# Optimization experiments

Measured on AMD Instinct MI355X. Metric: run time of the kernel, lower is better.

The kernel has to match this reference:

```python
import jax, jax.numpy as jnp
import numpy as np

STRIDE = 16
SIZES = np.array([128.0, 256.0, 512.0], np.float32)
RATIOS = np.array([0.5, 1.0, 2.0], np.float32)
N_POS, N_NEG = 32, 32          # n_sample=64, pos_ratio=0.5
POS_THR, NEG_THR = 0.7, 0.2
W_CONF, W_REG = 1.0, 5.0


def _conv(x, w, b, stride, pad):
    y = jax.lax.conv_general_dilated(x, w, (stride, stride), [(pad, pad), (pad, pad)],
                                     dimension_numbers=('NCHW', 'OIHW', 'NCHW'))
    return y + b[None, :, None, None]


def _anchors(fw, fh, stride):
    # 9 anchors per center: 3 sizes x 3 aspect ratios
    ws = (SIZES[:, None] * np.sqrt(RATIOS)[None, :]).reshape(-1)
    hs = (SIZES[:, None] / np.sqrt(RATIOS)[None, :]).reshape(-1)
    wh = jnp.asarray(np.stack([ws, hs], -1))                      # (9,2)
    cx = (jnp.arange(fw, dtype=jnp.float32) + 0.5) * stride
    cy = (jnp.arange(fh, dtype=jnp.float32) + 0.5) * stride
    gx, gy = jnp.meshgrid(cx, cy, indexing='ij')                  # x-major, like the torch list comp
    ctr = jnp.stack([gx, gy], -1)[:, :, None, :]                  # (fw,fh,1,2)
    tl = ctr - wh / 2.0
    xywh = jnp.concatenate([tl, jnp.broadcast_to(wh, tl.shape)], -1)  # (fw,fh,9,4)
    return xywh.reshape(-1, 4)


def _xywh_to_xyxy(b):
    return jnp.concatenate([b[:, :2], b[:, :2] + b[:, 2:]], -1)


def _iou(a, b):  # a [N,4], b [M,4], xyxy
    lt = jnp.maximum(a[:, None, :2], b[None, :, :2])
    rb = jnp.minimum(a[:, None, 2:], b[None, :, 2:])
    inter = jnp.clip(rb - lt, 0.0).prod(-1)
    aa = (a[:, 2] - a[:, 0]) * (a[:, 3] - a[:, 1])
    ab = (b[:, 2] - b[:, 0]) * (b[:, 3] - b[:, 1])
    return inter / (aa[:, None] + ab[None, :] - inter)


def _head_flat(y, per):  # [1, 9*per, H, W] -> [W*H*9, per], matching anchor flatten order
    _, _, H, W = y.shape
    return y[0].reshape(9, per, H, W).transpose(3, 2, 0, 1).reshape(-1, per)


def _apply_offsets(boxes, off):  # decode proposals from xyxy boxes + (dx,dy,dw,dh)
    w = boxes[:, 2] - boxes[:, 0]; h = boxes[:, 3] - boxes[:, 1]
    cx = boxes[:, 0] + 0.5 * w;    cy = boxes[:, 1] + 0.5 * h
    ncx = cx + off[:, 0] * w;      ncy = cy + off[:, 1] * h
    nw = w * jnp.exp(off[:, 2]);   nh = h * jnp.exp(off[:, 3])
    return jnp.stack([ncx - nw / 2, ncy - nh / 2, ncx + nw / 2, ncy + nh / 2], -1)


def _box_offset(anc, gt):
    aw = anc[:, 2] - anc[:, 0]; ah = anc[:, 3] - anc[:, 1]
    acx = anc[:, 0] + 0.5 * aw; acy = anc[:, 1] + 0.5 * ah
    gw = gt[:, 2] - gt[:, 0];   gh = gt[:, 3] - gt[:, 1]
    gcx = gt[:, 0] + 0.5 * gw;  gcy = gt[:, 1] + 0.5 * gh
    return jnp.stack([(gcx - acx) / aw, (gcy - acy) / ah,
                      jnp.log(gw / aw), jnp.log(gh / ah)], -1)


def setup_inputs():
    key = jax.random.key(0)
    ks = jax.random.split(key, 12)
    img_data = jax.random.normal(ks[0], (1, 3, 1600, 1600), jnp.float32)
    x1 = jax.random.uniform(ks[1], (64,), minval=0.0, maxval=1400.0)
    y1 = jax.random.uniform(ks[2], (64,), minval=0.0, maxval=1400.0)
    bw = jax.random.uniform(ks[3], (64,), minval=32.0, maxval=200.0)
    bh = jax.random.uniform(ks[4], (64,), minval=32.0, maxval=200.0)
    gt_boxes = jnp.stack([x1, y1, x1 + bw, y1 + bh], -1)[None]   # [1,64,4], all valid (no -1 pad)
    gt_classes = jax.random.randint(ks[5], (1, 64), 1, 21, jnp.int32)
    def w(k, shape, fan):
        return jax.random.normal(k, shape, jnp.float32) * np.float32(np.sqrt(2.0 / fan))
    return dict(
        img_data=img_data, gt_boxes=gt_boxes, gt_classes=gt_classes,
        w1=w(ks[6], (64, 3, 7, 7), 3 * 49),      b1=jnp.zeros(64, jnp.float32),
        w2=w(ks[7], (256, 64, 3, 3), 64 * 9),    b2=jnp.zeros(256, jnp.float32),
        w_rpn=w(ks[8], (256, 256, 3, 3), 256 * 9), b_rpn=jnp.zeros(256, jnp.float32),
        w_cls=w(ks[9], (18, 256, 1, 1), 256),    b_cls=jnp.zeros(18, jnp.float32),
        w_reg=w(ks[10], (36, 256, 1, 1), 256),   b_reg=jnp.zeros(36, jnp.float32),
    )


def reference(img_data, gt_boxes, gt_classes, w1, b1, w2, b2, w_rpn, b_rpn, w_cls, b_cls, w_reg, b_reg):
    # --- feature extractor (total stride 16) ---
    fm = jax.nn.relu(_conv(img_data, w1, b1, 4, 3))
    fm = jax.nn.relu(_conv(fm, w2, b2, 4, 1))            # [1,256,100,100]
    H, W = fm.shape[2], fm.shape[3]
    # --- anchors + IoU matching ---
    anchors_xywh = _anchors(W, H, STRIDE)                # [N,4] xywh
    anchors_xyxy = _xywh_to_xyxy(anchors_xywh)
    gt = gt_boxes[0]                                     # [M,4], all valid
    ious = _iou(anchors_xyxy, gt)                        # [N,M]
    N = ious.shape[0]
    gt_max = ious.max(0)                                 # best iou per gt
    is_gt_best = (ious == gt_max[None, :]).any(1)        # torch: where(iou == gt_max)[0]
    anc_argmax = ious.argmax(1)
    anc_max = ious.max(1)
    labels = jnp.full((N,), -1.0, jnp.float32)
    labels = jnp.where(anc_max < NEG_THR, 0.0, labels)
    labels = jnp.where(is_gt_best, 1.0, labels)
    labels = jnp.where(anc_max > POS_THR, 1.0, labels)
    # --- deterministic pos/neg sampling (fixed sizes; replaces randperm subsampling) ---
    idx = jnp.arange(N, dtype=jnp.float32)
    _, pos_index = jax.lax.top_k(jnp.where(labels == 1.0, anc_max, -1.0), N_POS)
    _, neg_index = jax.lax.top_k(jnp.where(labels == 0.0, 1e6 - idx, -1e9), N_NEG)
    bboxes_pos = anchors_xyxy[pos_index]                 # box_convert(xywh->xyxy) of pos anchors
    # --- proposal module (RPN head) ---
    h = jax.nn.relu(_conv(fm, w_rpn, b_rpn, 1, 1))
    cls = _head_flat(_conv(h, w_cls, b_cls, 1, 0), 2)    # [N,2]
    reg = _head_flat(_conv(h, w_reg, b_reg, 1, 0), 4)    # [N,4]
    pos_score = cls[pos_index]
    neg_score = cls[neg_index]
    offset_pos = reg[pos_index]
    proposals = _apply_offsets(bboxes_pos, offset_pos)
    # --- losses ---
    gt_offset = _box_offset(bboxes_pos, gt[anc_argmax[pos_index]])
    logits = jnp.concatenate([pos_score, neg_score], 0)  # [64,2]
    tgt = jnp.concatenate([jnp.ones(N_POS, jnp.int32), jnp.zeros(N_NEG, jnp.int32)])
    logp = jax.nn.log_softmax(logits, -1)
    cls_loss = -logp[jnp.arange(N_POS + N_NEG), tgt].mean()
    d = gt_offset - offset_pos
    ad = jnp.abs(d)
    reg_loss = jnp.where(ad < 1.0, 0.5 * d * d, ad - 0.5).mean()
    total_rpn_loss = W_CONF * cls_loss + W_REG * reg_loss
    gt_cls_pos = gt_classes[0][anc_argmax[pos_index]]
    return (total_rpn_loss, fm, proposals, pos_index, gt_cls_pos)
```

## Files before the change

kernel.cpp:

```cpp
#include <hip/hip_runtime.h>
#include <math.h>


#define CAP 4096

typedef __attribute__((ext_vector_type(8))) short bf16x8;
typedef __attribute__((ext_vector_type(4))) float f32x4;

__device__ __forceinline__ void dma16(const void* g, void* l) {
    __builtin_amdgcn_global_load_lds((const __attribute__((address_space(1))) void*)g,
                                     (__attribute__((address_space(3))) void*)l, 16, 0, 0);
}

#define OFF_F1T     0
#define OFF_FMT     5171328
#define OFF_CPART   6503040
#define OFF_RPART   7223040
#define OFF_WA1     8663040
#define OFF_W9_2    8672448
#define OFF_W9_3    8746176
#define OFF_WTC     9041088
#define OFF_WTG     9045696
#define OFF_AARG    9054912
#define OFF_NEGM    9144912
#define OFF_POSM    9147728
#define OFF_GTMAX   9150544
#define OFF_CANDS   9150688
#define OFF_CANDI   9154784
#define OFF_IMGB    9158880

__device__ __forceinline__ unsigned short f2bf(float f) {
    unsigned int u = __float_as_uint(f);
    u += 0x7fffu + ((u >> 16) & 1u);
    return (unsigned short)(u >> 16);
}

__device__ __forceinline__ void anchor_box(int i, float& x0, float& y0,
                                           float& x1, float& y1, float& area) {
#pragma clang fp contract(off)
    const float sizes[3]  = {128.f, 256.f, 512.f};
    const float ratios[3] = {0.5f, 1.f, 2.f};
    int a = i % 9;
    int q = i / 9;
    int iy = q % 100;
    int ix = q / 100;
    int s = a / 3, r = a % 3;
    float sq = sqrtf(ratios[r]);
    float w = sizes[s] * sq;
    float h = sizes[s] / sq;
    float cx = ((float)ix + 0.5f) * 16.0f;
    float cy = ((float)iy + 0.5f) * 16.0f;
    x0 = cx - w * 0.5f;
    y0 = cy - h * 0.5f;
    x1 = x0 + w;
    y1 = y0 + h;
    area = (x1 - x0) * (y1 - y0);
}

__device__ __forceinline__ float iou_one(float ax0, float ay0, float ax1, float ay1, float aa,
                                         float bx0, float by0, float bx1, float by1, float ab) {
#pragma clang fp contract(off)
    float ltx = fmaxf(ax0, bx0), lty = fmaxf(ay0, by0);
    float rbx = fminf(ax1, bx1), rby = fminf(ay1, by1);
    float iw = fmaxf(rbx - ltx, 0.0f);
    float ih = fmaxf(rby - lty, 0.0f);
    float inter = iw * ih;
    return inter / ((aa + ab) - inter);
}

__global__ __launch_bounds__(256) void setup_kernel(const float* __restrict__ wc, float* __restrict__ wtc,
                                                    const float* __restrict__ wg, float* __restrict__ wtg,
                                                    const float* __restrict__ w1, unsigned short* __restrict__ wa1,
                                                    const float* __restrict__ w2, unsigned short* __restrict__ w9_2,
                                                    const float* __restrict__ wr, unsigned short* __restrict__ w9_3,
                                                    unsigned int* __restrict__ f1t_u, unsigned int* __restrict__ fmt_u,
                                                    unsigned int* __restrict__ gtmax,
                                                    const float* __restrict__ img, unsigned short* __restrict__ imgb) {
    int i = blockIdx.x * 256 + threadIdx.x;
    if (i < 65) { gtmax[i] = 0u; return; }
    i -= 65;
    if (i < 103040) {
        if (i < 51328) {
            int p = i >> 5, part = i & 31;
            int x, y;
            if (p < 804) { y = (p < 402) ? 0 : 401; x = p % 402; }
            else { int j = p - 804; x = (j < 400) ? 0 : 401; y = 1 + (j % 400); }
            f1t_u[(y * 402 + x) * 32 + part] = 0u;
        } else {
            int i2 = i - 51328;
            int p = i2 >> 7, part = i2 & 127;
            int x, y;
            if (p < 204) { y = (p < 102) ? 0 : 101; x = p % 102; }
            else { int j = p - 204; x = (j < 100) ? 0 : 101; y = 1 + (j % 100); }
            fmt_u[(y * 102 + x) * 128 + part] = 0u;
        }
        return;
    }
    i -= 103040;
    if (i < 4608) { int c = i / 256, k = i - c * 256; wtc[k * 18 + c] = wc[i]; return; }
    i -= 4608;
    if (i < 9216) { int c = i / 256, k = i - c * 256; wtg[k * 36 + c] = wg[i]; return; }
    i -= 9216;
    if (i < 12288) {
        int oc = i / 192, k = i - oc * 192;
        int q = k >> 3, kx = k & 7;
        int ky = q / 3, ic = q - (q / 3) * 3;
        wa1[i] = (q < 21 && kx < 7) ? f2bf(w1[oc * 147 + ic * 49 + ky * 7 + kx])
                                    : (unsigned short)0;
        return;
    }
    i -= 12288;
    if (i < 147456) {
        int unit = i >> 13;
        int rem = i & 8191;
        int ocT = rem >> 9;
        int rem2 = rem & 511;
        int lane = rem2 >> 3;
        int e = rem2 & 7;
        int cc = unit >> 1, kcl = unit & 1;
        int oc = ocT * 16 + (lane & 15);
        int ic = kcl * 32 + (lane >> 4) * 8 + e;
        w9_2[i] = f2bf(w2[(oc * 64 + ic) * 9 + cc]);
        return;
    }
    i -= 147456;
    if (i < 589824) {
        int unit = i >> 13;
        int rem = i & 8191;
        int ocT = rem >> 9;
        int rem2 = rem & 511;
        int lane = rem2 >> 3;
        int e = rem2 & 7;
        int cc = unit >> 1, kcl = unit & 1;
        int kk = cc >> 2, chv = cc & 3;
        int oc = ocT * 16 + (lane & 15);
        int icl = kcl * 32 + (lane >> 4) * 8 + e;
        w9_3[i] = f2bf(wr[(oc * 256 + chv * 64 + icl) * 9 + kk]);
        return;
    }
    i -= 589824;
    if (i < 7680000) {
        int ic = i / 2560000;
        int rem = i - ic * 2560000;
        int y = rem / 1600, x = rem - (rem / 1600) * 1600;
        imgb[((size_t)(ic * 1608 + y + 3)) * 1608 + x + 3] = f2bf(img[((size_t)(ic * 1600 + y)) * 1600 + x]);
        return;
    }
    i -= 7680000;
    if (i < 38592) {
        int ic = i / 12864;
        int rem = i - ic * 12864;
        int r8 = rem / 1608, xp = rem - r8 * 1608;
        int yp = (r8 < 3) ? r8 : (1600 + r8);
        imgb[((size_t)(ic * 1608 + yp)) * 1608 + xp] = 0;
        return;
    }
    i -= 38592;
    if (i < 28800) {
        int ic = i / 9600;
        int rem = i - ic * 9600;
        int y = rem / 6, xi = rem - (rem / 6) * 6;
        int xp = (xi < 3) ? xi : (1602 + xi);
        imgb[((size_t)(ic * 1608 + y + 3)) * 1608 + xp] = 0;
    }
}

__device__ __forceinline__ void iou1_body(int bid, int t, const float* __restrict__ gt,
                                          int* __restrict__ aarg, unsigned int* __restrict__ gtmax) {
    __shared__ float sg1[64][4];
    __shared__ float sarea1[64];
    __shared__ unsigned int smax1[64];
    if (t < 64) {
#pragma clang fp contract(off)
        float b0 = gt[t * 4 + 0], b1 = gt[t * 4 + 1];
        float b2 = gt[t * 4 + 2], b3 = gt[t * 4 + 3];
        sg1[t][0] = b0; sg1[t][1] = b1; sg1[t][2] = b2; sg1[t][3] = b3;
        sarea1[t] = (b2 - b0) * (b3 - b1);
        smax1[t] = 0u;
    }
    __syncthreads();
    int i = bid * 256 + t;
    int iq = min(i, 89999);
    float x0, y0, x1, y1, aa;
    anchor_box(iq, x0, y0, x1, y1, aa);
    float best = -1.f;
    int bestj = 0;
    for (int j = 0; j < 64; j++) {
        float v = iou_one(x0, y0, x1, y1, aa, sg1[j][0], sg1[j][1], sg1[j][2], sg1[j][3], sarea1[j]);
        if (v > best) { best = v; bestj = j; }
        float vm = v;
#pragma unroll
        for (int off = 32; off > 0; off >>= 1) vm = fmaxf(vm, __shfl_xor(vm, off));
        if ((t & 63) == 0) atomicMax(&smax1[j], __float_as_uint(vm));
    }
    if (i < 90000) aarg[i] = bestj;
    __syncthreads();
    if (t < 64) atomicMax(&gtmax[t], smax1[t]);
}

__device__ __forceinline__ void iou2_body(int bid, int t, const float* __restrict__ gt,
                                          const unsigned int* __restrict__ gtmax,
                                          unsigned long long* __restrict__ negmask,
                                          unsigned long long* __restrict__ posmask,
                                          float* __restrict__ cand_s, int* __restrict__ cand_i,
                                          unsigned int* __restrict__ cnt) {
    __shared__ float sg2[64][4];
    __shared__ float sarea2[64];
    __shared__ float sgm2[64];
    if (t < 64) {
#pragma clang fp contract(off)
        float b0 = gt[t * 4 + 0], b1 = gt[t * 4 + 1];
        float b2 = gt[t * 4 + 2], b3 = gt[t * 4 + 3];
        sg2[t][0] = b0; sg2[t][1] = b1; sg2[t][2] = b2; sg2[t][3] = b3;
        sarea2[t] = (b2 - b0) * (b3 - b1);
        sgm2[t] = __uint_as_float(gtmax[t]);
    }
    __syncthreads();
    int i = bid * 512 + t;
    if (i >= 90000) return;
    float x0, y0, x1, y1, aa;
    anchor_box(i, x0, y0, x1, y1, aa);
    float best = -1.f;
    bool isbest = false;
    for (int j = 0; j < 64; j++) {
        float v = iou_one(x0, y0, x1, y1, aa, sg2[j][0], sg2[j][1], sg2[j][2], sg2[j][3], sarea2[j]);
        if (v > best) best = v;
        if (v == sgm2[j]) isbest = true;
    }
    float label = -1.f;
    if (best < 0.2f) label = 0.f;
    if (isbest) label = 1.f;
    if (best > 0.7f) label = 1.f;
    unsigned long long negb = __ballot(label == 0.f);
    unsigned long long posb = __ballot(label == 1.f);
    if ((t & 63) == 0) { negmask[i >> 6] = negb; posmask[i >> 6] = posb; }
    if (label == 1.f) {
        unsigned int p = atomicAdd(cnt, 1u);
        if (p < CAP) { cand_s[p] = best; cand_i[p] = i; }
    }
}

__device__ __forceinline__ void conv1_body(int bx, int oy, int t,
                                           const unsigned short* __restrict__ imgb,
                                           const unsigned short* __restrict__ wA,
                                           const float* __restrict__ bias,
                                           unsigned short* __restrict__ f1t) {
    __shared__ __align__(16) unsigned char smem[13312];
    unsigned short* win = (unsigned short*)smem;
    unsigned short* tileT = (unsigned short*)smem;
    int wave = t >> 6, lane = t & 63;
    int quad = lane >> 4, l16 = lane & 15;
    int ox0 = bx * 64;
    int col0 = ox0 * 4;
    int gy0 = 4 * oy - 3;
    const size_t ZROW = ((size_t)(2 * 1608 + 1606)) * 1608;

    for (int o = wave; o < 13; o += 4) {
        int q = o * 64 + lane;
        int r = q / 33;
        int c = q - r * 33;
        int rc = min(r, 20);
        int ky = rc / 3, ic = rc - (rc / 3) * 3;
        int yp = gy0 + ky + 3;
        size_t offm = ((size_t)(ic * 1608 + yp)) * 1608 + col0 + c * 8;
        size_t offz = ZROW + (size_t)(q - 693) * 8;
        dma16(imgb + ((r < 21) ? offm : offz), (char*)smem + o * 1024);
    }
    bf16x8 afr[6];
    {
        const bf16x8* ap = (const bf16x8*)(wA + (wave * 16 + l16) * 192 + quad * 8);
#pragma unroll
        for (int c = 0; c < 6; c++) afr[c] = ap[c * 4];
    }
    __syncthreads();

    f32x4 acc[4];
#pragma unroll
    for (int j = 0; j < 4; j++) acc[j] = (f32x4){0.f, 0.f, 0.f, 0.f};
#pragma unroll
    for (int ch = 0; ch < 6; ch++) {
        const unsigned short* wrow = win + (ch * 4 + quad) * 264;
#pragma unroll
        for (int j = 0; j < 4; j++) {
            int px = j * 16 + l16;
            const unsigned long long* bp = (const unsigned long long*)(wrow + 4 * px);
            union { unsigned long long u[2]; bf16x8 v; } uu;
            uu.u[0] = bp[0];
            uu.u[1] = bp[1];
            acc[j] = __builtin_amdgcn_mfma_f32_16x16x32_bf16(afr[ch], uu.v, acc[j], 0, 0, 0);
        }
    }
    __syncthreads();
#pragma unroll
    for (int reg = 0; reg < 4; reg++) {
        int oc = wave * 16 + quad * 4 + reg;
        float bv = bias[oc];
#pragma unroll
        for (int j = 0; j < 4; j++) {
            int px = j * 16 + l16;
            tileT[px * 72 + oc] = f2bf(fmaxf(acc[j][reg] + bv, 0.f));
        }
    }
    __syncthreads();
    int px = t >> 2, part = t & 3;
    int ox = ox0 + px;
    if (ox < 400) {
        int row = (oy + 1) * 402 + ox + 1;
        uint4 v0 = *(const uint4*)(tileT + px * 72 + part * 16);
        uint4 v1 = *(const uint4*)(tileT + px * 72 + part * 16 + 8);
        *(uint4*)(f1t + row * 64 + part * 16) = v0;
        *(uint4*)(f1t + row * 64 + part * 16 + 8) = v1;
    }
}

__global__ __launch_bounds__(256, 4) void conv1_iou1(const unsigned short* __restrict__ imgb,
                                                     const unsigned short* __restrict__ wA,
                                                     const float* __restrict__ bias,
                                                     unsigned short* __restrict__ f1t,
                                                     const float* __restrict__ gt,
                                                     int* __restrict__ aarg,
                                                     unsigned int* __restrict__ gtmax) {
    int t = threadIdx.x;
    if (blockIdx.x < 7) {
        conv1_body(blockIdx.x, blockIdx.y, t, imgb, wA, bias, f1t);
    } else {
        int bid = blockIdx.y;
        if (bid < 352) iou1_body(bid, t, gt, aarg, gtmax);
    }
}

template<int ICC, int RS, int S, bool WRT, bool HEAD>
__device__ __forceinline__ void conv_body(int xs, int y, int t,
                                          const unsigned short* __restrict__ Bt,
                                          const unsigned short* __restrict__ A9,
                                          const float* __restrict__ bias,
                                          float* __restrict__ outF,
                                          unsigned short* __restrict__ outT,
                                          const float* __restrict__ wtc,
                                          const float* __restrict__ wtg,
                                          float* __restrict__ cpart,
                                          float* __restrict__ rpart) {
    constexpr int NC = ICC / 64;
    constexpr int HC = S * 24 + 3;
    constexpr int CHW = ICC / 8;
    constexpr int TOT = 3 * HC * CHW;
    constexpr int BOPS = (TOT + 63) / 64;
    constexpr int BB = BOPS * 1024;
    constexpr int NS = (NC == 1) ? 18 : 72;
    __shared__ __align__(16) unsigned char smem[BB + 32768];
    unsigned short* blds = (unsigned short*)smem;
    float* hlds = (float*)(smem + BB);

    int wave = t >> 6, lane = t & 63;
    int ow = wave & 3, ph = wave >> 2;
    int quad = lane >> 4, l16 = lane & 15;
    int oc0 = ow * 64;
    int pl = ph * 16 + l16;
    int pxe = min(pl, 24);
    int swp = pxe & 7;

    for (int o = wave; o < BOPS; o += 8) {
        int q = min(o * 64 + lane, TOT - 1);
        int row = q / CHW;
        int e = q - row * CHW;
        int ky = row / HC;
        int c = row - ky * HC;
        int sz = (S == 4) ? (e ^ ((c >> 2) & 7)) : (e ^ (row & 7));
        dma16(Bt + ((size_t)(S * y + ky) * RS + S * xs * 25 + c) * ICC + sz * 8,
              (char*)smem + o * 1024);
    }
    for (int o = wave; o < 16; o += 8)
        dma16(A9 + (size_t)(o * 64 + lane) * 8, (char*)smem + BB + o * 1024);

    f32x4 acc[4];
#pragma unroll
    for (int mt = 0; mt < 4; mt++) acc[mt] = (f32x4){0.f, 0.f, 0.f, 0.f};
    __syncthreads();

    for (int u = 0; u < NS; u++) {
        if (u + 1 < NS) {
            char* dst = (char*)smem + BB + ((u + 1) & 1) * 16384;
            const unsigned short* src = A9 + (size_t)(u + 1) * 8192;
            for (int o = wave; o < 16; o += 8)
                dma16(src + (size_t)(o * 64 + lane) * 8, dst + o * 1024);
        }
        const unsigned short* ab = (const unsigned short*)(smem + BB + (u & 1) * 16384);
        int cc = u >> 1, kcl = u & 1;
        int pass = cc / NC, ch = cc - pass * NC;
        int ky = pass / 3, kx = pass - (pass / 3) * 3;
        int row = ky * HC + S * pxe + kx;
        int ck = kcl * 4 + quad;
        int chunk = (S == 4) ? (ck ^ swp) : ((ch * 8 + ck) ^ (row & 7));
        bf16x8 bf = *(const bf16x8*)(blds + row * ICC + chunk * 8);
#pragma unroll
        for (int mt = 0; mt < 4; mt++) {
            bf16x8 af = *(const bf16x8*)(ab + ((ow * 4 + mt) * 64 + lane) * 8);
            acc[mt] = __builtin_amdgcn_mfma_f32_16x16x32_bf16(af, bf, acc[mt], 0, 0, 0);
        }
        __syncthreads();
    }

#pragma unroll
    for (int mt = 0; mt < 4; mt++) {
#pragma unroll
        for (int reg = 0; reg < 4; reg++) {
            int oc = oc0 + mt * 16 + quad * 4 + reg;
            float bv = bias[oc];
            if (pl < 25) {
                float v = fmaxf(acc[mt][reg] + bv, 0.f);
                if (HEAD) {
                    hlds[oc * 26 + pl] = v;
                } else {
                    int p = y * 100 + xs * 25 + pl;
                    outF[oc * 10000 + p] = v;
                    if (WRT) {
                        int r = (y + 1) * 102 + xs * 25 + pl + 1;
                        outT[r * 256 + oc] = f2bf(v);
                    }
                }
            }
        }
    }
    if (HEAD) {
        __syncthreads();
        int base = y * 100 + xs * 25;
        for (int it = t; it < 5400; it += 512) {
            int ch = it / 1350;
            int r = it - ch * 1350;
            int j = r / 25;
            int p = r - j * 25;
            int jc = (j < 18) ? j : (j - 18);
            const float* wt = (j < 18) ? (wtc + jc) : (wtg + jc);
            int stride = (j < 18) ? 18 : 36;
            int ic0 = ch * 64;
            float acc2 = 0.f;
#pragma unroll 8
            for (int ic = 0; ic < 64; ic++)
                acc2 += hlds[(ic0 + ic) * 26 + p] * wt[(ic0 + ic) * stride];
            float* dst = (j < 18) ? (cpart + (ch * 18 + jc) * 10000)
                                  : (rpart + (ch * 36 + jc) * 10000);
            dst[base + p] = acc2;
        }
    }
}

__global__ __launch_bounds__(512, 4) void conv2_iou2(const unsigned short* __restrict__ Bt,
                                                     const unsigned short* __restrict__ A9,
                                                     const float* __restrict__ bias,
                                                     float* __restrict__ outF,
                                                     unsigned short* __restrict__ outT,
                                                     const float* __restrict__ gt,
                                                     const unsigned int* __restrict__ gtmax,
                                                     unsigned long long* __restrict__ negmask,
                                                     unsigned long long* __restrict__ posmask,
                                                     float* __restrict__ cand_s,
                                                     int* __restrict__ cand_i,
                                                     unsigned int* __restrict__ cnt) {
    int t = threadIdx.x;
    if (blockIdx.x < 4) {
        conv_body<64, 402, 4, true, false>(blockIdx.x, blockIdx.y, t, Bt, A9, bias,
                                           outF, outT, nullptr, nullptr, nullptr, nullptr);
    } else {
        int bid = (blockIdx.x - 4) * 100 + blockIdx.y;
        if (bid < 176) iou2_body(bid, t, gt, gtmax, negmask, posmask, cand_s, cand_i, cnt);
    }
}

__global__ __launch_bounds__(512, 4) void conv3_head(const unsigned short* __restrict__ Bt,
                                                     const unsigned short* __restrict__ A9,
                                                     const float* __restrict__ bias,
                                                     const float* __restrict__ wtc,
                                                     const float* __restrict__ wtg,
                                                     float* __restrict__ cpart,
                                                     float* __restrict__ rpart) {
    conv_body<256, 102, 1, false, true>(blockIdx.x, blockIdx.y, threadIdx.x, Bt, A9, bias,
                                        nullptr, nullptr, wtc, wtg, cpart, rpart);
}

__device__ __forceinline__ unsigned long long shflx64(unsigned long long v, int m) {
    int lo = __shfl_xor((int)(unsigned)(v & 0xFFFFFFFFull), m);
    int hi = __shfl_xor((int)(unsigned)(v >> 32), m);
    return ((unsigned long long)(unsigned)hi << 32) | (unsigned)lo;
}

__device__ int wave_first32(const unsigned long long* __restrict__ mask,
                            bool invert, int* __restrict__ outIdx, int lane) {
    const int NW = 1407;
    const int WPT = 22;
    unsigned long long mw[WPT];
    int cnt = 0;
#pragma unroll
    for (int u = 0; u < WPT; u++) {
        int w = lane * WPT + u;
        unsigned long long m = 0ull;
        if (w < NW) {
            m = mask[w];
            if (invert) m = ~m;
            if (w == NW - 1) m &= 0xFFFFull;
        }
        mw[u] = m;
        cnt += __builtin_popcountll(m);
    }
    int inc = cnt;
#pragma unroll
    for (int off = 1; off < 64; off <<= 1) {
        int v = __shfl_up(inc, off);
        if (lane >= off) inc += v;
    }
    int total = __shfl(inc, 63);
    int pref = inc - cnt;
    if (pref < 32) {
#pragma unroll
        for (int u = 0; u < WPT; u++) {
            unsigned long long m = mw[u];
            int wbase = (lane * WPT + u) * 64;
            while (m && pref < 32) {
                int b = __builtin_ctzll(m);
                outIdx[pref++] = wbase + b;
                m &= m - 1;
            }
        }
    }
    return total;
}

__global__ __launch_bounds__(64) void tail_kernel(const unsigned long long* __restrict__ negmask,
                                                  const unsigned long long* __restrict__ posmask,
                                                  const float* __restrict__ cand_s,
                                                  const int* __restrict__ cand_i,
                                                  const unsigned int* __restrict__ cnt,
                                                  const float* __restrict__ cpart,
                                                  const float* __restrict__ rpart,
                                                  const float* __restrict__ bcls,
                                                  const float* __restrict__ breg,
                                                  const int* __restrict__ aarg,
                                                  const float* __restrict__ gt,
                                                  const int* __restrict__ gtc,
                                                  float* __restrict__ out) {
    __shared__ unsigned long long keys[CAP + 32];
    __shared__ int sfill[32];
    __shared__ int spidx[32];
    __shared__ int snidx[32];
    int lane = threadIdx.x;

    int ncand = min((int)*cnt, CAP);
    for (int c = lane; c < ncand; c += 64) {
        unsigned u = __float_as_uint(cand_s[c]);
        u ^= (u & 0x80000000u) ? 0xFFFFFFFFu : 0x80000000u;
        keys[c] = ((unsigned long long)u << 32) | (0xFFFFFFFFu - (unsigned)cand_i[c]);
    }
    int ntot = ncand;
    if (ncand < 32) {
        int tot = wave_first32(posmask, true, sfill, lane);
        int nfill = min(tot, 32);
        unsigned um1 = __float_as_uint(-1.0f) ^ 0xFFFFFFFFu;
        for (int k2 = lane; k2 < nfill; k2 += 64)
            keys[ncand + k2] = ((unsigned long long)um1 << 32) | (0xFFFFFFFFu - (unsigned)sfill[k2]);
        ntot += nfill;
    }

    unsigned long long lk = 0ull; int ls = -1;
    for (int c = lane; c < ntot; c += 64) {
        unsigned long long k = keys[c];
        if (k > lk) { lk = k; ls = c; }
    }
    for (int s = 0; s < 32; s++) {
        unsigned long long mk = lk;
#pragma unroll
        for (int off = 1; off < 64; off <<= 1) {
            unsigned long long o = shflx64(mk, off);
            if (o > mk) mk = o;
        }
        if (lk == mk && mk != 0ull) {
            spidx[s] = (int)(0xFFFFFFFFu - (unsigned)(mk & 0xFFFFFFFFull));
            keys[ls] = 0ull;
            lk = 0ull; ls = -1;
            for (int c = lane; c < ntot; c += 64) {
                unsigned long long k = keys[c];
                if (k > lk) { lk = k; ls = c; }
            }
        }
    }

    int totn = wave_first32(negmask, false, snidx, lane);
    if (lane == 0) {
        int nf = min(totn, 32);
        for (int s = nf; s < 32; s++) snidx[s] = s;
    }

    {
#pragma clang fp contract(off)
        const int PROP_OFF = 1 + 2560000;
        int t = lane;
        int n = (t < 32) ? spidx[t] : snidx[t - 32];
        int a = n % 9;
        int q = n / 9;
        int iy = q % 100;
        int ix = q / 100;
        int p = iy * 100 + ix;

        float l0 = bcls[a * 2 + 0], l1 = bcls[a * 2 + 1];
        for (int c = 0; c < 4; c++) {
            l0 += cpart[(c * 18 + a * 2 + 0) * 10000 + p];
            l1 += cpart[(c * 18 + a * 2 + 1) * 10000 + p];
        }
        float m = fmaxf(l0, l1);
        float lse = m + logf(expf(l0 - m) + expf(l1 - m));
        float logp = ((t < 32) ? l1 : l0) - lse;
        float cls_sum = logp;
#pragma unroll
        for (int off = 32; off > 0; off >>= 1) cls_sum += __shfl_down(cls_sum, off);

        float reg_sum = 0.f;
        if (t < 32) {
            float offv[4];
#pragma unroll
            for (int k = 0; k < 4; k++) {
                float v = breg[a * 4 + k];
                for (int c = 0; c < 4; c++) v += rpart[(c * 36 + a * 4 + k) * 10000 + p];
                offv[k] = v;
            }
            float x0, y0, x1, y1, aa;
            anchor_box(n, x0, y0, x1, y1, aa);
            float w = x1 - x0, h = y1 - y0;
            float cx = x0 + 0.5f * w, cy = y0 + 0.5f * h;
            float ncx = cx + offv[0] * w, ncy = cy + offv[1] * h;
            float nw = w * expf(offv[2]), nh = h * expf(offv[3]);
            out[PROP_OFF + t * 4 + 0] = ncx - nw * 0.5f;
            out[PROP_OFF + t * 4 + 1] = ncy - nh * 0.5f;
            out[PROP_OFF + t * 4 + 2] = ncx + nw * 0.5f;
            out[PROP_OFF + t * 4 + 3] = ncy + nh * 0.5f;

            int j = aarg[n];
            float g0 = gt[j * 4 + 0], g1 = gt[j * 4 + 1];
            float g2 = gt[j * 4 + 2], g3 = gt[j * 4 + 3];
            float gw = g2 - g0, gh = g3 - g1;
            float gcx = g0 + 0.5f * gw, gcy = g1 + 0.5f * gh;
            float tg[4];
            tg[0] = (gcx - cx) / w;
            tg[1] = (gcy - cy) / h;
            tg[2] = logf(gw / w);
            tg[3] = logf(gh / h);
#pragma unroll
            for (int k = 0; k < 4; k++) {
                float d = tg[k] - offv[k];
                float ad = fabsf(d);
                reg_sum += (ad < 1.f) ? 0.5f * d * d : ad - 0.5f;
            }
            out[PROP_OFF + 128 + t] = (float)n;
            out[PROP_OFF + 160 + t] = (float)gtc[j];
        }
#pragma unroll
        for (int off = 32; off > 0; off >>= 1) reg_sum += __shfl_down(reg_sum, off);
        if (t == 0) {
            float cls_loss = -(cls_sum / 64.f);
            float reg_loss = reg_sum / 128.f;
            out[0] = cls_loss + 5.f * reg_loss;
        }
    }
}

extern "C" void kernel_launch(void* const* d_in, const int* in_sizes, int n_in,
                              void* d_out, int out_size, void* d_ws, size_t ws_size,
                              hipStream_t stream) {
    const float* img = (const float*)d_in[0];
    const float* gt  = (const float*)d_in[1];
    const int*   gtc = (const int*)d_in[2];
    const float* w1  = (const float*)d_in[3];
    const float* b1  = (const float*)d_in[4];
    const float* w2  = (const float*)d_in[5];
    const float* b2  = (const float*)d_in[6];
    const float* wr  = (const float*)d_in[7];
    const float* br  = (const float*)d_in[8];
    const float* wc  = (const float*)d_in[9];
    const float* bc  = (const float*)d_in[10];
    const float* wg  = (const float*)d_in[11];
    const float* bg  = (const float*)d_in[12];
    float* out = (float*)d_out;
    float* ws = (float*)d_ws;

    unsigned short* f1t  = (unsigned short*)(ws + OFF_F1T);
    unsigned short* fmt  = (unsigned short*)(ws + OFF_FMT);
    unsigned short* wa1  = (unsigned short*)(ws + OFF_WA1);
    unsigned short* w9_2 = (unsigned short*)(ws + OFF_W9_2);
    unsigned short* w9_3 = (unsigned short*)(ws + OFF_W9_3);
    unsigned short* imgb = (unsigned short*)(ws + OFF_IMGB);
    float* cpart = ws + OFF_CPART;
    float* rpart = ws + OFF_RPART;
    float* wtc   = ws + OFF_WTC;
    float* wtg   = ws + OFF_WTG;
    int*   aarg  = (int*)(ws + OFF_AARG);
    unsigned long long* negm = (unsigned long long*)(ws + OFF_NEGM);
    unsigned long long* posm = (unsigned long long*)(ws + OFF_POSM);
    unsigned int* gtmax = (unsigned int*)(ws + OFF_GTMAX);
    unsigned int* cnt   = gtmax + 64;
    float* cands = ws + OFF_CANDS;
    int*   candi = (int*)(ws + OFF_CANDI);
    float* fm    = out + 1;

    setup_kernel<<<dim3(33649), dim3(256), 0, stream>>>(wc, wtc, wg, wtg, w1, wa1,
                                                        w2, w9_2, wr, w9_3,
                                                        (unsigned int*)f1t, (unsigned int*)fmt, gtmax,
                                                        img, imgb);

    conv1_iou1<<<dim3(8, 400), dim3(256), 0, stream>>>(imgb, wa1, b1, f1t, gt, aarg, gtmax);
    conv2_iou2<<<dim3(6, 100), dim3(512), 0, stream>>>(f1t, w9_2, b2, fm, fmt,
                                                       gt, gtmax, negm, posm, cands, candi, cnt);
    conv3_head<<<dim3(4, 100), dim3(512), 0, stream>>>(fmt, w9_3, br, wtc, wtg, cpart, rpart);
    tail_kernel<<<dim3(1), dim3(64), 0, stream>>>(negm, posm, cands, candi, cnt,
                                                  cpart, rpart, bc, bg, aarg, gt, gtc, out);
}
```

Baseline: 303.1 us.

## Vectorize image padding, triple-buffer conv weight loads, simplify IoU max reduction

Rewrites the setup image conversion so each thread packs 8 bf16 values into one 16-byte store with padding folded in, eliminating the separate border-zeroing passes and shrinking the grid. The conv weight staging becomes a three-stage ring with prefetch distance two and explicit vmcnt waits plus a raw barrier, reducing per-iteration full syncs. The IoU per-gt max uses a guarded shared atomic instead of a wave shuffle reduction. The occupancy hint is dropped and LDS grows, which may lower occupancy.

```diff
diff --git a/kernel.cpp b/kernel.cpp
--- a/kernel.cpp
+++ b/kernel.cpp
@@ -139,29 +139,30 @@
         return;
     }
     i -= 589824;
-    if (i < 7680000) {
-        int ic = i / 2560000;
-        int rem = i - ic * 2560000;
-        int y = rem / 1600, x = rem - (rem / 1600) * 1600;
-        imgb[((size_t)(ic * 1608 + y + 3)) * 1608 + x + 3] = f2bf(img[((size_t)(ic * 1600 + y)) * 1600 + x]);
-        return;
-    }
-    i -= 7680000;
-    if (i < 38592) {
-        int ic = i / 12864;
-        int rem = i - ic * 12864;
-        int r8 = rem / 1608, xp = rem - r8 * 1608;
-        int yp = (r8 < 3) ? r8 : (1600 + r8);
-        imgb[((size_t)(ic * 1608 + yp)) * 1608 + xp] = 0;
-        return;
-    }
-    i -= 38592;
-    if (i < 28800) {
-        int ic = i / 9600;
-        int rem = i - ic * 9600;
-        int y = rem / 6, xi = rem - (rem / 6) * 6;
-        int xp = (xi < 3) ? xi : (1602 + xi);
-        imgb[((size_t)(ic * 1608 + y + 3)) * 1608 + xp] = 0;
+    if (i < 974448) {
+        int ic = i / 324816;
+        int rem = i - ic * 324816;
+        int row = rem / 202;
+        int k = rem - row * 202;
+        int y = row - 3;
+        bool yok = (y >= 0) && (y < 1600);
+        int yc = min(max(y, 0), 1599);
+        const float* srow = img + ((size_t)(ic * 1600 + yc)) * 1600;
+        unsigned int d[4];
+#pragma unroll
+        for (int e2 = 0; e2 < 4; e2++) {
+            int x0 = k * 8 + 2 * e2 - 11;
+            int x1 = x0 + 1;
+            bool ok0 = yok && (x0 >= 0) && (x0 < 1600);
+            bool ok1 = yok && (x1 >= 0) && (x1 < 1600);
+            float f0 = srow[min(max(x0, 0), 1599)];
+            float f1 = srow[min(max(x1, 0), 1599)];
+            unsigned int lo = ok0 ? (unsigned int)f2bf(f0) : 0u;
+            unsigned int hi = ok1 ? (unsigned int)f2bf(f1) : 0u;
+            d[e2] = lo | (hi << 16);
+        }
+        *(uint4*)(imgb + ((size_t)(ic * 1608 + row)) * 1616 + k * 8) =
+            make_uint4(d[0], d[1], d[2], d[3]);
     }
 }
 
@@ -188,10 +189,7 @@
     for (int j = 0; j < 64; j++) {
         float v = iou_one(x0, y0, x1, y1, aa, sg1[j][0], sg1[j][1], sg1[j][2], sg1[j][3], sarea1[j]);
         if (v > best) { best = v; bestj = j; }
-        float vm = v;
-#pragma unroll
-        for (int off = 32; off > 0; off >>= 1) vm = fmaxf(vm, __shfl_xor(vm, off));
-        if ((t & 63) == 0) atomicMax(&smax1[j], __float_as_uint(vm));
+        if (v > __uint_as_float(smax1[j])) atomicMax(&smax1[j], __float_as_uint(v));
     }
     if (i < 90000) aarg[i] = bestj;
     __syncthreads();
@@ -251,9 +249,8 @@
     int wave = t >> 6, lane = t & 63;
     int quad = lane >> 4, l16 = lane & 15;
     int ox0 = bx * 64;
-    int col0 = ox0 * 4;
+    int col0 = ox0 * 4 + 8;
     int gy0 = 4 * oy - 3;
-    const size_t ZROW = ((size_t)(2 * 1608 + 1606)) * 1608;
 
     for (int o = wave; o < 13; o += 4) {
         int q = o * 64 + lane;
@@ -262,8 +259,8 @@
         int rc = min(r, 20);
         int ky = rc / 3, ic = rc - (rc / 3) * 3;
         int yp = gy0 + ky + 3;
-        size_t offm = ((size_t)(ic * 1608 + yp)) * 1608 + col0 + c * 8;
-        size_t offz = ZROW + (size_t)(q - 693) * 8;
+        size_t offm = ((size_t)(ic * 1608 + yp)) * 1616 + col0 + c * 8;
+        size_t offz = (size_t)(q - 693) * 8;
         dma16(imgb + ((r < 21) ? offm : offz), (char*)smem + o * 1024);
     }
     bf16x8 afr[6];
@@ -347,7 +344,7 @@
     constexpr int BOPS = (TOT + 63) / 64;
     constexpr int BB = BOPS * 1024;
     constexpr int NS = (NC == 1) ? 18 : 72;
-    __shared__ __align__(16) unsigned char smem[BB + 32768];
+    __shared__ __align__(16) unsigned char smem[BB + 49152];
     unsigned short* blds = (unsigned short*)smem;
     float* hlds = (float*)(smem + BB);
 
@@ -369,8 +366,17 @@
         dma16(Bt + ((size_t)(S * y + ky) * RS + S * xs * 25 + c) * ICC + sz * 8,
               (char*)smem + o * 1024);
     }
-    for (int o = wave; o < 16; o += 8)
-        dma16(A9 + (size_t)(o * 64 + lane) * 8, (char*)smem + BB + o * 1024);
+    {
+        char* s0 = (char*)smem + BB;
+        dma16(A9 + (size_t)(wave * 64 + lane) * 8, s0 + wave * 1024);
+        dma16(A9 + (size_t)((wave + 8) * 64 + lane) * 8, s0 + (wave + 8) * 1024);
+        if (NS > 1) {
+            char* s1 = (char*)smem + BB + 16384;
+            const unsigned short* a1 = A9 + 8192;
+            dma16(a1 + (size_t)(wave * 64 + lane) * 8, s1 + wave * 1024);
+            dma16(a1 + (size_t)((wave + 8) * 64 + lane) * 8, s1 + (wave + 8) * 1024);
+        }
+    }
 
     f32x4 acc[4];
 #pragma unroll
@@ -378,13 +384,7 @@
     __syncthreads();
 
     for (int u = 0; u < NS; u++) {
-        if (u + 1 < NS) {
-            char* dst = (char*)smem + BB + ((u + 1) & 1) * 16384;
-            const unsigned short* src = A9 + (size_t)(u + 1) * 8192;
-            for (int o = wave; o < 16; o += 8)
-                dma16(src + (size_t)(o * 64 + lane) * 8, dst + o * 1024);
-        }
-        const unsigned short* ab = (const unsigned short*)(smem + BB + (u & 1) * 16384);
+        const unsigned short* ab = (const unsigned short*)(smem + BB + (u % 3) * 16384);
         int cc = u >> 1, kcl = u & 1;
         int pass = cc / NC, ch = cc - pass * NC;
         int ky = pass / 3, kx = pass - (pass / 3) * 3;
@@ -397,8 +397,21 @@
             bf16x8 af = *(const bf16x8*)(ab + ((ow * 4 + mt) * 64 + lane) * 8);
             acc[mt] = __builtin_amdgcn_mfma_f32_16x16x32_bf16(af, bf, acc[mt], 0, 0, 0);
         }
-        __syncthreads();
-    }
+        if (u + 2 < NS) {
+            char* dst = (char*)smem + BB + ((u + 2) % 3) * 16384;
+            const unsigned short* src = A9 + (size_t)(u + 2) * 8192;
+            dma16(src + (size_t)(wave * 64 + lane) * 8, dst + wave * 1024);
+            dma16(src + (size_t)((wave + 8) * 64 + lane) * 8, dst + (wave + 8) * 1024);
+        }
+        if (u + 1 < NS) {
+            if (u + 2 < NS) asm volatile("s_waitcnt vmcnt(2)" ::: "memory");
+            else            asm volatile("s_waitcnt vmcnt(0)" ::: "memory");
+            __builtin_amdgcn_s_barrier();
+            __builtin_amdgcn_sched_barrier(0);
+        }
+    }
+
+    if (HEAD) __syncthreads();
 
 #pragma unroll
     for (int mt = 0; mt < 4; mt++) {
@@ -444,18 +457,18 @@
     }
 }
 
-__global__ __launch_bounds__(512, 4) void conv2_iou2(const unsigned short* __restrict__ Bt,
-                                                     const unsigned short* __restrict__ A9,
-                                                     const float* __restrict__ bias,
-                                                     float* __restrict__ outF,
-                                                     unsigned short* __restrict__ outT,
-                                                     const float* __restrict__ gt,
-                                                     const unsigned int* __restrict__ gtmax,
-                                                     unsigned long long* __restrict__ negmask,
-                                                     unsigned long long* __restrict__ posmask,
-                                                     float* __restrict__ cand_s,
-                                                     int* __restrict__ cand_i,
-                                                     unsigned int* __restrict__ cnt) {
+__global__ __launch_bounds__(512) void conv2_iou2(const unsigned short* __restrict__ Bt,
+                                                  const unsigned short* __restrict__ A9,
+                                                  const float* __restrict__ bias,
+                                                  float* __restrict__ outF,
+                                                  unsigned short* __restrict__ outT,
+                                                  const float* __restrict__ gt,
+                                                  const unsigned int* __restrict__ gtmax,
+                                                  unsigned long long* __restrict__ negmask,
+                                                  unsigned long long* __restrict__ posmask,
+                                                  float* __restrict__ cand_s,
+                                                  int* __restrict__ cand_i,
+                                                  unsigned int* __restrict__ cnt) {
     int t = threadIdx.x;
     if (blockIdx.x < 4) {
         conv_body<64, 402, 4, true, false>(blockIdx.x, blockIdx.y, t, Bt, A9, bias,
@@ -466,13 +479,13 @@
     }
 }
 
-__global__ __launch_bounds__(512, 4) void conv3_head(const unsigned short* __restrict__ Bt,
-                                                     const unsigned short* __restrict__ A9,
-                                                     const float* __restrict__ bias,
-                                                     const float* __restrict__ wtc,
-                                                     const float* __restrict__ wtg,
-                                                     float* __restrict__ cpart,
-                                                     float* __restrict__ rpart) {
+__global__ __launch_bounds__(512) void conv3_head(const unsigned short* __restrict__ Bt,
+                                                  const unsigned short* __restrict__ A9,
+                                                  const float* __restrict__ bias,
+                                                  const float* __restrict__ wtc,
+                                                  const float* __restrict__ wtg,
+                                                  float* __restrict__ cpart,
+                                                  float* __restrict__ rpart) {
     conv_body<256, 102, 1, false, true>(blockIdx.x, blockIdx.y, threadIdx.x, Bt, A9, bias,
                                         nullptr, nullptr, wtc, wtg, cpart, rpart);
 }
@@ -698,10 +711,10 @@
     int*   candi = (int*)(ws + OFF_CANDI);
     float* fm    = out + 1;
 
-    setup_kernel<<<dim3(33649), dim3(256), 0, stream>>>(wc, wtc, wg, wtg, w1, wa1,
-                                                        w2, w9_2, wr, w9_3,
-                                                        (unsigned int*)f1t, (unsigned int*)fmt, gtmax,
-                                                        img, imgb);
+    setup_kernel<<<dim3(7192), dim3(256), 0, stream>>>(wc, wtc, wg, wtg, w1, wa1,
+                                                       w2, w9_2, wr, w9_3,
+                                                       (unsigned int*)f1t, (unsigned int*)fmt, gtmax,
+                                                       img, imgb);
 
     conv1_iou1<<<dim3(8, 400), dim3(256), 0, stream>>>(imgb, wa1, b1, f1t, gt, aarg, gtmax);
     conv2_iou2<<<dim3(6, 100), dim3(512), 0, stream>>>(f1t, w9_2, b2, fm, fmt,
```

New measurement: 306.1 us. Within noise of the previous version (+1.0%).
